# Optimization experiments

Hardware: AMD Instinct MI355X
Metric: run time of the kernel (lower is better)

## Reference

```python
import jax, jax.numpy as jnp
import numpy as np

# iRPE contextual+transposed, method=PRODUCT, rpe config ratio=1.9
ALPHA, BETA, GAMMA = 1.9, 3.8, 15.2
BETA_INT = int(BETA)            # 3
S = 2 * BETA_INT + 1            # 7
NUM_BUCKETS = S * S             # 49
B, H, D = 8, 8, 64
HEIGHT = WIDTH = 32
L = HEIGHT * WIDTH              # 1024, skip = L - height*width = 0


def _piecewise_index(rp):
    # numpy port of torch piecewise_index (no-grad, precomputed constant)
    rp = np.asarray(rp)
    rp_abs = np.abs(rp)
    safe = np.maximum(rp_abs.astype(np.float64), ALPHA)  # avoid log(0) under mask
    y = ALPHA + np.log(safe / ALPHA) / np.log(GAMMA / ALPHA) * (BETA - ALPHA)
    y = np.minimum(np.round(y), BETA)                    # round then clip(max=beta)
    out = np.where(rp_abs <= ALPHA, np.round(rp.astype(np.float64)), np.sign(rp) * y)
    return out.astype(np.int64)                          # trunc toward zero (+-3.8 -> +-3)


def _rp_bucket_product(height, width):
    pos = np.stack(np.meshgrid(np.arange(height), np.arange(width), indexing='ij'), -1)
    pos = pos.reshape(-1, 2)                             # (L, 2)
    diff = pos[:, None, :] - pos[None, :, :]             # (L, L, 2)
    r = _piecewise_index(diff[:, :, 0]) + BETA_INT
    c = _piecewise_index(diff[:, :, 1]) + BETA_INT
    return (r * S + c).astype(np.int32)                  # values in [0, 49)


def setup_inputs() -> dict:
    key = jax.random.key(0)
    k1, k2 = jax.random.split(key)
    x = jax.random.normal(k1, (B, H, L, D), dtype=jnp.float32)
    lookup_table_weight = jax.random.normal(k2, (H, D, NUM_BUCKETS), dtype=jnp.float32) * 0.02
    rp_bucket = jnp.asarray(_rp_bucket_product(HEIGHT, WIDTH))  # (L, L) int32 constant
    return {"x": x, "lookup_table_weight": lookup_table_weight, "rp_bucket": rp_bucket}


def reference(x, lookup_table_weight, rp_bucket):
    # x: (B, H, L, D); lookup_table_weight: (H, D, K); rp_bucket: (L, L) int
    # lt[b,h,l,k] = sum_d x[b,h,l,d] * W[h,d,k]
    lt = jnp.einsum('bhld,hdk->bhlk', x, lookup_table_weight)  # (B, H, L, K) small
    Lq = rp_bucket.shape[0]
    row = jnp.arange(Lq)[:, None]                              # (L, 1)
    # out[b,h,i,j] = lt[b,h,i,rp_bucket[i,j]] -- the big irregular gather
    return lt[:, :, row, rp_bucket]                            # (B, H, L, L)
```

## Files before the change

### kernel.cpp

```cpp
#include <hip/hip_runtime.h>


constexpr int cL = 1024;
constexpr int cD = 64;
constexpr int cK = 49;
constexpr int cHALF = 32;

typedef float vf4 __attribute__((ext_vector_type(4)));

__global__ __launch_bounds__(256) void irpe_fused(
    const float* __restrict__ x,
    const float* __restrict__ W,
    const int*   __restrict__ bucket,
    float*       __restrict__ out)
{
    __shared__ vf4  xs4[cHALF][cD / 4];
    __shared__ float lts[cHALF * cK];

    const int gid  = blockIdx.x;
    const int i    = gid >> 1;
    const int bh0  = (gid & 1) * cHALF;
    const int tid  = threadIdx.x;

    const vf4* x4 = (const vf4*)x;
    #pragma unroll
    for (int r = 0; r < 2; ++r) {
        const int idx = r * 256 + tid;
        const int lh  = idx >> 4;
        const int d4  = idx & 15;
        xs4[lh][d4] = __builtin_nontemporal_load(
            &x4[((size_t)(bh0 + lh) * cL + i) * (cD / 4) + d4]);
    }

    const int4 bk = ((const int4*)(bucket + (size_t)i * cL))[tid];

    __syncthreads();

    const float* xsf = (const float*)xs4;
    for (int p = tid; p < cHALF * cK; p += 256) {
        const int lh = p / cK;
        const int k  = p - lh * cK;
        const int h  = (bh0 + lh) & 7;
        const float* wp = W + (size_t)h * cD * cK + k;
        const float* xr = xsf + lh * cD;
        float acc = 0.0f;
        #pragma unroll
        for (int d = 0; d < cD; ++d) {
            acc = fmaf(xr[d], wp[(size_t)d * cK], acc);
        }
        lts[p] = acc;
    }
    __syncthreads();

    vf4* obase = (vf4*)(out + ((size_t)bh0 * cL + i) * cL);
    #pragma unroll 4
    for (int lh = 0; lh < cHALF; ++lh) {
        const float* lrow = lts + lh * cK;
        vf4 o;
        o.x = lrow[bk.x];
        o.y = lrow[bk.y];
        o.z = lrow[bk.z];
        o.w = lrow[bk.w];
        __builtin_nontemporal_store(o, &obase[(size_t)lh * cL * (cL / 4) + tid]);
    }
}

extern "C" void kernel_launch(void* const* d_in, const int* in_sizes, int n_in,
                              void* d_out, int out_size, void* d_ws, size_t ws_size,
                              hipStream_t stream) {
    const float* x      = (const float*)d_in[0];
    const float* W      = (const float*)d_in[1];
    const int*   bucket = (const int*)d_in[2];
    float*       out    = (float*)d_out;

    const int grid = cL * 2;
    irpe_fused<<<grid, 256, 0, stream>>>(x, W, bucket, out);
}
```

Before: 311.0 us.

## Split batch-head work into quarters, swizzle block-to-row mapping, vectorize x reads

Each block now handles 16 batch-heads instead of 32, which doubles the grid to 4096 blocks and halves per-block shared memory and work. Blocks are mapped to query rows with a bit-swizzle so that consecutive blocks touch different i values. The inner dot product now reads x from shared memory as float4, and launch bounds request 8 blocks per CU. The aim is higher occupancy and better spread of the write-bound output stores, at the cost of loading each bucket row twice as often.

```diff
diff --git a/kernel.cpp b/kernel.cpp
--- a/kernel.cpp
+++ b/kernel.cpp
@@ -4,57 +4,58 @@
 constexpr int cL = 1024;
 constexpr int cD = 64;
 constexpr int cK = 49;
-constexpr int cHALF = 32;
+constexpr int BG = 16;
 
 typedef float vf4 __attribute__((ext_vector_type(4)));
 
-__global__ __launch_bounds__(256) void irpe_fused(
+__global__ __launch_bounds__(256, 8) void irpe_fused(
     const float* __restrict__ x,
     const float* __restrict__ W,
     const int*   __restrict__ bucket,
     float*       __restrict__ out)
 {
-    __shared__ vf4  xs4[cHALF][cD / 4];
-    __shared__ float lts[cHALF * cK];
+    __shared__ float xs[BG][cD];
+    __shared__ float lts[BG * cK];
 
-    const int gid  = blockIdx.x;
-    const int i    = gid >> 1;
-    const int bh0  = (gid & 1) * cHALF;
-    const int tid  = threadIdx.x;
+    const int gid     = blockIdx.x;
+    const int quarter = gid & 3;
+    const int i_lo    = (gid >> 8) & 7;
+    const int i_hi    = ((gid >> 11) & 1) * 64 + ((gid >> 2) & 63);
+    const int i       = i_hi * 8 + i_lo;
+    const int bh0     = quarter * BG;
+    const int tid     = threadIdx.x;
 
-    const vf4* x4 = (const vf4*)x;
-    #pragma unroll
-    for (int r = 0; r < 2; ++r) {
-        const int idx = r * 256 + tid;
-        const int lh  = idx >> 4;
-        const int d4  = idx & 15;
-        xs4[lh][d4] = __builtin_nontemporal_load(
-            &x4[((size_t)(bh0 + lh) * cL + i) * (cD / 4) + d4]);
+    {
+        const int lh = tid >> 4;
+        const int d4 = tid & 15;
+        ((vf4*)xs[lh])[d4] = __builtin_nontemporal_load(
+            &((const vf4*)x)[((size_t)(bh0 + lh) * cL + i) * (cD / 4) + d4]);
     }
-
     const int4 bk = ((const int4*)(bucket + (size_t)i * cL))[tid];
-
     __syncthreads();
 
-    const float* xsf = (const float*)xs4;
-    for (int p = tid; p < cHALF * cK; p += 256) {
+    for (int p = tid; p < BG * cK; p += 256) {
         const int lh = p / cK;
         const int k  = p - lh * cK;
-        const int h  = (bh0 + lh) & 7;
+        const int h  = lh & 7;
         const float* wp = W + (size_t)h * cD * cK + k;
-        const float* xr = xsf + lh * cD;
+        const vf4* xr4 = (const vf4*)xs[lh];
         float acc = 0.0f;
         #pragma unroll
-        for (int d = 0; d < cD; ++d) {
-            acc = fmaf(xr[d], wp[(size_t)d * cK], acc);
+        for (int d4 = 0; d4 < cD / 4; ++d4) {
+            const vf4 xv = xr4[d4];
+            acc = fmaf(xv.x, wp[(d4 * 4 + 0) * cK], acc);
+            acc = fmaf(xv.y, wp[(d4 * 4 + 1) * cK], acc);
+            acc = fmaf(xv.z, wp[(d4 * 4 + 2) * cK], acc);
+            acc = fmaf(xv.w, wp[(d4 * 4 + 3) * cK], acc);
         }
         lts[p] = acc;
     }
     __syncthreads();
 
-    vf4* obase = (vf4*)(out + ((size_t)bh0 * cL + i) * cL);
+    vf4* obase = (vf4*)out + ((size_t)bh0 * cL + i) * (cL / 4);
     #pragma unroll 4
-    for (int lh = 0; lh < cHALF; ++lh) {
+    for (int lh = 0; lh < BG; ++lh) {
         const float* lrow = lts + lh * cK;
         vf4 o;
         o.x = lrow[bk.x];
@@ -73,6 +74,6 @@
     const int*   bucket = (const int*)d_in[2];
     float*       out    = (float*)d_out;
 
-    const int grid = cL * 2;
+    const int grid = cL * 4;
     irpe_fused<<<grid, 256, 0, stream>>>(x, W, bucket, out);
 }
```

Result: slower. 360.3 us (+15.9%).
